# Kernel optimization log

Measured on AMD Instinct MI355X. Metric: run time of the kernel, lower is better.

## Reference

```python
import jax, jax.numpy as jnp
import numpy as np

N_NODES = 2048
D = 1024
B = 16384
E = 65536

def setup_inputs() -> dict:
    key = jax.random.key(0)
    ks = jax.random.split(key, 8)
    feat = jax.random.normal(ks[0], (B, 7, D), dtype=jnp.float32)
    data_x = jax.random.randint(ks[1], (7 * B,), 0, N_NODES, dtype=jnp.int64)
    adj_rows = jnp.sort(jax.random.randint(ks[2], (E,), 0, N_NODES, dtype=jnp.int32))
    adj_cols = jax.random.randint(ks[3], (E,), 0, N_NODES, dtype=jnp.int32)
    adj_vals = jax.random.uniform(ks[4], (E,), dtype=jnp.float32)
    # kaiming-uniform-like init for GCN weights, zero bias (as in reset_parameters)
    def kaiming(k, fan_in, fan_out):
        bound = jnp.sqrt(6.0 / fan_in)
        return jax.random.uniform(k, (fan_in, fan_out), minval=-bound, maxval=bound, dtype=jnp.float32)
    W1 = kaiming(ks[5], D, N_NODES)
    W2 = kaiming(ks[6], N_NODES, N_NODES)
    W3 = kaiming(ks[7], N_NODES, D)
    return {"feat": feat, "data_x": data_x, "adj_rows": adj_rows, "adj_cols": adj_cols,
            "adj_vals": adj_vals, "W1": W1, "b1": jnp.zeros((N_NODES,), jnp.float32),
            "W2": W2, "b2": jnp.zeros((N_NODES,), jnp.float32),
            "W3": W3, "b3": jnp.zeros((D,), jnp.float32)}

def reference(feat, data_x, adj_rows, adj_cols, adj_vals, W1, b1, W2, b2, W3, b3):
    n = b1.shape[0]  # number of nodes N
    e1 = data_x[0::7]  # [B]
    e2 = data_x[1::7]  # [B]
    # scatter-add: adjacency_matrix[e1] += feat[i,0]; adjacency_matrix[e2] += feat[i,1]
    idx = jnp.concatenate([e1, e2])                       # [2B]
    vals = jnp.concatenate([feat[:, 0, :], feat[:, 1, :]])  # [2B, D]
    node_feat = jax.ops.segment_sum(vals, idx, num_segments=n)  # [N, D]

    def spmm(x):  # sparse [N,N] @ dense [N,F]
        return jax.ops.segment_sum(adj_vals[:, None] * x[adj_cols], adj_rows, num_segments=n)

    h = jax.nn.relu(spmm(node_feat @ W1) + b1)  # [N, N]
    h = spmm(h @ W2) + b2                        # [N, N]
    logits = spmm(h @ W3) + b3                   # [N, D]

    # gather then swap: feat[:,0]=logits[e2], feat[:,1]=logits[e1]
    out = jnp.concatenate([logits[e2][:, None, :], logits[e1][:, None, :], feat[:, 2:, :]], axis=1)
    return out
```

## Files before the change

kernel.cpp:

```cpp
#include <hip/hip_runtime.h>
#include <stdint.h>

#define N_NODES 2048
#define DIM 1024
#define BATCH 16384
#define NEDGE 65536
#define CAP 96

typedef __bf16 bf16x8 __attribute__((ext_vector_type(8)));
typedef float f32x4 __attribute__((ext_vector_type(4)));
typedef unsigned short u16;
typedef unsigned int u32;

__device__ __forceinline__ float bf2f(u16 u) {
  union { u32 i; float f; } v; v.i = ((u32)u) << 16; return v.f;
}
__device__ __forceinline__ u16 f2bf(float f) {
  union { float f; u32 i; } v; v.f = f;
  u32 r = v.i + 0x7fffu + ((v.i >> 16) & 1u);
  return (u16)(r >> 16);
}

__global__ void k_detect(const int* __restrict__ dx, int* __restrict__ flag,
                         int* __restrict__ counts) {
  int t = threadIdx.x;
  for (int j = t; j < N_NODES; j += 64) counts[j] = 0;
  if (t == 0) {
    int is64 = 1;
    for (int j = 0; j < 32; ++j)
      if (dx[2 * j + 1] != 0) { is64 = 0; break; }
    *flag = is64;
  }
}

__global__ __launch_bounds__(256) void k_bucket(const int* __restrict__ dx,
                                                const int* __restrict__ flag,
                                                int* __restrict__ counts,
                                                int* __restrict__ bucket) {
  int i = blockIdx.x * 256 + threadIdx.x;
  if (i >= 2 * BATCH) return;
  int f = *flag;
  long p = (i < BATCH) ? 7L * i : 7L * (i - BATCH) + 1;
  int n = dx[f ? 2 * p : p] & (N_NODES - 1);
  int slot = atomicAdd(&counts[n], 1);
  if (slot < CAP) bucket[n * CAP + slot] = i;
}

__global__ __launch_bounds__(256) void k_nodesum(const float* __restrict__ feat,
                                                 const int* __restrict__ counts,
                                                 const int* __restrict__ bucket,
                                                 u16* __restrict__ A1) {
  int n = blockIdx.x;
  int tid = threadIdx.x;
  int cnt = counts[n]; if (cnt > CAP) cnt = CAP;
  float a0 = 0.f, a1 = 0.f, a2 = 0.f, a3 = 0.f;
  for (int j = 0; j < cnt; ++j) {
    int i = bucket[n * CAP + j];
    size_t rowoff = (i < BATCH) ? ((size_t)i * 7) * DIM
                                : ((size_t)(i - BATCH) * 7 + 1) * DIM;
    f32x4 v = *(const f32x4*)(feat + rowoff + tid * 4);
    a0 += v[0]; a1 += v[1]; a2 += v[2]; a3 += v[3];
  }
  ushort4 o; o.x = f2bf(a0); o.y = f2bf(a1); o.z = f2bf(a2); o.w = f2bf(a3);
  *(ushort4*)(A1 + (size_t)n * DIM + tid * 4) = o;
}

__global__ __launch_bounds__(256) void k_transpose(const float* __restrict__ W,
                                                   u16* __restrict__ Wt,
                                                   int K, int N) {
  __shared__ __align__(16) u16 t[32][33];
  int ntx = N >> 5;
  int bx = blockIdx.x % ntx;
  int by = blockIdx.x / ntx;
  int tx = threadIdx.x & 31, ty = threadIdx.x >> 5;
  #pragma unroll
  for (int r = 0; r < 32; r += 8)
    t[r + ty][tx] = f2bf(W[(size_t)(by * 32 + r + ty) * N + bx * 32 + tx]);
  __syncthreads();
  #pragma unroll
  for (int r = 0; r < 32; r += 8)
    Wt[(size_t)(bx * 32 + r + ty) * K + by * 32 + tx] = t[tx][r + ty];
}

__global__ __launch_bounds__(256) void k_rowptr(const int* __restrict__ adj_rows,
                                                int* __restrict__ row_ptr) {
  int r = blockIdx.x * 256 + threadIdx.x;
  if (r > N_NODES) return;
  int lo = 0, hi = NEDGE;
  while (lo < hi) { int mid = (lo + hi) >> 1; if (adj_rows[mid] < r) lo = mid + 1; else hi = mid; }
  row_ptr[r] = lo;
}

__global__ __launch_bounds__(256) void k_spmm(const u16* __restrict__ X16,
                                              const int* __restrict__ row_ptr,
                                              const int* __restrict__ adj_cols,
                                              const float* __restrict__ adj_vals,
                                              const float* __restrict__ bias,
                                              u16* __restrict__ Y16,
                                              float* __restrict__ Y32,
                                              int width) {
  int chunks = width >> 10;
  int ch = blockIdx.x % chunks;
  int r = blockIdx.x / chunks;
  int col = ch * 1024 + threadIdx.x * 4;
  int e0 = row_ptr[r], e1 = row_ptr[r + 1];
  float a0 = 0.f, a1 = 0.f, a2 = 0.f, a3 = 0.f;
  int e = e0;
  for (; e + 2 <= e1; e += 2) {
    int c0 = adj_cols[e] & (N_NODES - 1);
    int c1 = adj_cols[e + 1] & (N_NODES - 1);
    float v0 = adj_vals[e], v1 = adj_vals[e + 1];
    ushort4 x0 = *(const ushort4*)(X16 + (size_t)c0 * width + col);
    ushort4 x1 = *(const ushort4*)(X16 + (size_t)c1 * width + col);
    a0 += v0 * bf2f(x0.x) + v1 * bf2f(x1.x);
    a1 += v0 * bf2f(x0.y) + v1 * bf2f(x1.y);
    a2 += v0 * bf2f(x0.z) + v1 * bf2f(x1.z);
    a3 += v0 * bf2f(x0.w) + v1 * bf2f(x1.w);
  }
  if (e < e1) {
    int c = adj_cols[e] & (N_NODES - 1);
    float v = adj_vals[e];
    ushort4 x = *(const ushort4*)(X16 + (size_t)c * width + col);
    a0 += v * bf2f(x.x); a1 += v * bf2f(x.y);
    a2 += v * bf2f(x.z); a3 += v * bf2f(x.w);
  }
  if (Y16) {
    ushort4 o; o.x = f2bf(a0); o.y = f2bf(a1); o.z = f2bf(a2); o.w = f2bf(a3);
    *(ushort4*)(Y16 + (size_t)r * width + col) = o;
  } else {
    f32x4 bb = *(const f32x4*)(bias + col);
    f32x4 o; o[0] = a0 + bb[0]; o[1] = a1 + bb[1]; o[2] = a2 + bb[2]; o[3] = a3 + bb[3];
    *(f32x4*)(Y32 + (size_t)r * width + col) = o;
  }
}

template <int BM, int BN, bool BIAS, bool RELU>
__global__ __launch_bounds__(256) void k_gemm(const u16* __restrict__ A,
                                              const u16* __restrict__ Bt,
                                              const float* __restrict__ bias,
                                              u16* __restrict__ C16,
                                              int M, int N, int K) {
  constexpr int BK = 64;
  constexpr int WM = BM / 2, WN = BN / 2;
  constexpr int MI = WM / 16, NI = WN / 16;
  constexpr int IA = BM / 32, IB = BN / 32;
  __shared__ __align__(16) u16 As[2][BM * BK];
  __shared__ __align__(16) u16 Bs[2][BN * BK];
  const int ntx = N / BN;
  const int bx = blockIdx.x % ntx;
  const int by = blockIdx.x / ntx;
  const int tid = threadIdx.x;
  const int wid = tid >> 6;
  const int lane = tid & 63;
  const int wr = wid >> 1, wc = wid & 1;
  const int rowbase = by * BM, colbase = bx * BN;

  f32x4 acc[MI][NI];
  #pragma unroll
  for (int i = 0; i < MI; ++i)
    #pragma unroll
    for (int j = 0; j < NI; ++j) acc[i][j] = (f32x4){0.f, 0.f, 0.f, 0.f};

  const int srow = tid >> 3;
  const int skk = (((tid & 7) ^ (srow & 7)) << 3);

  #define STAGE(buf, kt)                                                        \
    do {                                                                        \
      _Pragma("unroll")                                                         \
      for (int i = 0; i < IA; ++i) {                                            \
        const u16* g = A + (size_t)(rowbase + i * 32 + srow) * K + (kt) + skk;  \
        __builtin_amdgcn_global_load_lds(                                       \
            (const __attribute__((address_space(1))) u32*)g,                    \
            (__attribute__((address_space(3))) u32*)(&As[buf][i * 2048 + tid * 8]), \
            16, 0, 0);                                                          \
      }                                                                         \
      _Pragma("unroll")                                                         \
      for (int i = 0; i < IB; ++i) {                                            \
        const u16* g = Bt + (size_t)(colbase + i * 32 + srow) * K + (kt) + skk; \
        __builtin_amdgcn_global_load_lds(                                       \
            (const __attribute__((address_space(1))) u32*)g,                    \
            (__attribute__((address_space(3))) u32*)(&Bs[buf][i * 2048 + tid * 8]), \
            16, 0, 0);                                                          \
      }                                                                         \
    } while (0)

  const int rrow = lane & 15;
  const int kq = (lane >> 4) * 8;
  const int rswz = (lane & 7) << 3;

  const int nk = K >> 6;
  STAGE(0, 0);
  __syncthreads();

  for (int t = 0; t < nk; ++t) {
    const u16* as = As[t & 1];
    const u16* bs = Bs[t & 1];
    if (t + 1 < nk) STAGE((t + 1) & 1, (t + 1) << 6);
    bf16x8 af[MI][2], bfr[NI][2];
    #pragma unroll
    for (int mi = 0; mi < MI; ++mi) {
      int r = wr * WM + mi * 16 + rrow;
      #pragma unroll
      for (int h = 0; h < 2; ++h)
        af[mi][h] = *(const bf16x8*)(as + r * 64 + ((h * 32 + kq) ^ rswz));
    }
    #pragma unroll
    for (int ni = 0; ni < NI; ++ni) {
      int c = wc * WN + ni * 16 + rrow;
      #pragma unroll
      for (int h = 0; h < 2; ++h)
        bfr[ni][h] = *(const bf16x8*)(bs + c * 64 + ((h * 32 + kq) ^ rswz));
    }
    #pragma unroll
    for (int h = 0; h < 2; ++h)
      #pragma unroll
      for (int mi = 0; mi < MI; ++mi)
        #pragma unroll
        for (int ni = 0; ni < NI; ++ni)
          acc[mi][ni] = __builtin_amdgcn_mfma_f32_16x16x32_bf16(af[mi][h], bfr[ni][h], acc[mi][ni], 0, 0, 0);
    __syncthreads();
  }
  #undef STAGE

  #pragma unroll
  for (int mi = 0; mi < MI; ++mi) {
    #pragma unroll
    for (int ni = 0; ni < NI; ++ni) {
      int col = colbase + wc * WN + ni * 16 + rrow;
      float bv = BIAS ? bias[col] : 0.f;
      #pragma unroll
      for (int j = 0; j < 4; ++j) {
        int row = rowbase + wr * WM + mi * 16 + (lane >> 4) * 4 + j;
        float v = acc[mi][ni][j] + bv;
        if (RELU) v = fmaxf(v, 0.f);
        C16[(size_t)row * N + col] = f2bf(v);
      }
    }
  }
}

__global__ __launch_bounds__(256) void k_assemble(const float* __restrict__ feat,
                                                  const float* __restrict__ logits,
                                                  const int* __restrict__ dx,
                                                  const int* __restrict__ flag,
                                                  float* __restrict__ out) {
  int i = blockIdx.x;
  int b = i / 7, slot = i - b * 7;
  const float* src;
  if (slot <= 1) {
    int f = *flag;
    long p = 7L * b + (slot == 0 ? 1 : 0);
    int node = dx[f ? 2 * p : p] & (N_NODES - 1);
    src = logits + (size_t)node * DIM;
  } else {
    src = feat + ((size_t)b * 7 + slot) * DIM;
  }
  f32x4 v = *(const f32x4*)(src + threadIdx.x * 4);
  __builtin_nontemporal_store(v, (f32x4*)(out + ((size_t)b * 7 + slot) * DIM + threadIdx.x * 4));
}

extern "C" void kernel_launch(void* const* d_in, const int* in_sizes, int n_in,
                              void* d_out, int out_size, void* d_ws, size_t ws_size,
                              hipStream_t stream) {
  const float* feat   = (const float*)d_in[0];
  const int* data_x   = (const int*)d_in[1];
  const int* adj_rows = (const int*)d_in[2];
  const int* adj_cols = (const int*)d_in[3];
  const float* adj_vals = (const float*)d_in[4];
  const float* W1 = (const float*)d_in[5];
  const float* b1 = (const float*)d_in[6];
  const float* W2 = (const float*)d_in[7];
  const float* b2 = (const float*)d_in[8];
  const float* W3 = (const float*)d_in[9];
  const float* b3 = (const float*)d_in[10];
  float* out = (float*)d_out;

  char* ws = (char*)d_ws;
  size_t off = 0;
  auto alloc = [&](size_t bytes) {
    char* p = ws + off; off += (bytes + 511) & ~(size_t)511; return p;
  };
  int*  flag    = (int*)alloc(4);
  int*  counts  = (int*)alloc(N_NODES * 4);
  int*  bucket  = (int*)alloc((size_t)N_NODES * CAP * 4);
  int*  row_ptr = (int*)alloc((N_NODES + 1) * 4);
  u16*  A1      = (u16*)alloc((size_t)N_NODES * DIM * 2);
  u16*  S       = (u16*)alloc((size_t)N_NODES * N_NODES * 2);
  u16*  H       = (u16*)alloc((size_t)N_NODES * N_NODES * 2);
  u16*  X3      = (u16*)alloc((size_t)N_NODES * DIM * 2);
  u16*  Wt      = (u16*)alloc((size_t)N_NODES * N_NODES * 2);
  float* logits = (float*)alloc((size_t)N_NODES * DIM * 4);

  k_detect<<<1, 64, 0, stream>>>(data_x, flag, counts);
  k_bucket<<<(2 * BATCH + 255) / 256, 256, 0, stream>>>(data_x, flag, counts, bucket);
  k_nodesum<<<N_NODES, 256, 0, stream>>>(feat, counts, bucket, A1);
  k_rowptr<<<N_NODES / 256 + 1, 256, 0, stream>>>(adj_rows, row_ptr);

  k_transpose<<<(N_NODES / 32) * (DIM / 32), 256, 0, stream>>>(W1, Wt, DIM, N_NODES);
  k_spmm<<<N_NODES * (DIM / 1024), 256, 0, stream>>>(A1, row_ptr, adj_cols, adj_vals, nullptr, S, nullptr, DIM);
  k_gemm<128, 64, true, true><<<(N_NODES / 128) * (N_NODES / 64), 256, 0, stream>>>(S, Wt, b1, H, N_NODES, N_NODES, DIM);
  k_transpose<<<(N_NODES / 32) * (N_NODES / 32), 256, 0, stream>>>(W2, Wt, N_NODES, N_NODES);
  k_spmm<<<N_NODES * (N_NODES / 1024), 256, 0, stream>>>(H, row_ptr, adj_cols, adj_vals, nullptr, S, nullptr, N_NODES);
  k_gemm<128, 64, true, false><<<(N_NODES / 128) * (N_NODES / 64), 256, 0, stream>>>(S, Wt, b2, H, N_NODES, N_NODES, N_NODES);
  k_transpose<<<(DIM / 32) * (N_NODES / 32), 256, 0, stream>>>(W3, Wt, N_NODES, DIM);
  k_gemm<64, 64, false, false><<<(N_NODES / 64) * (DIM / 64), 256, 0, stream>>>(H, Wt, nullptr, X3, N_NODES, DIM, N_NODES);
  k_spmm<<<N_NODES * (DIM / 1024), 256, 0, stream>>>(X3, row_ptr, adj_cols, adj_vals, b3, nullptr, logits, DIM);

  k_assemble<<<BATCH * 7, 256, 0, stream>>>(feat, logits, data_x, flag, out);
}
```

Before: 322.9 us.

## Overlap feat passthrough copy with GEMM/SpMM kernels and scatter logits directly

Splits the passthrough copy of feat slots 2..6 into chunks that extra blocks appended to each GEMM and SpMM launch perform. This overlaps that memory-bound work with the compute-bound kernels. The final SpMM writes logits straight into the output rows through the node buckets, which removes the logits buffer and the gather pass. Row_ptr is folded into k_detect, and the three weight transposes are merged into one launch with separate buffers. The risk is that copy blocks compete for bandwidth and CU slots with the main kernels, and the bucket CAP cap could drop rows if any node has more than 96 hits.

```diff
diff --git a/kernel.cpp b/kernel.cpp
--- a/kernel.cpp
+++ b/kernel.cpp
@@ -21,15 +21,35 @@
   return (u16)(r >> 16);
 }
 
-__global__ void k_detect(const int* __restrict__ dx, int* __restrict__ flag,
-                         int* __restrict__ counts) {
+__device__ __forceinline__ void copy_feat_rows(const float* __restrict__ feat,
+                                               float* __restrict__ out,
+                                               int row0, int tid) {
+  #pragma unroll 4
+  for (int t = row0; t < row0 + 32; ++t) {
+    int b = t / 5, s = t - b * 5 + 2;
+    size_t o = ((size_t)b * 7 + s) * DIM + tid * 4;
+    f32x4 v = __builtin_nontemporal_load((const f32x4*)(feat + o));
+    __builtin_nontemporal_store(v, (f32x4*)(out + o));
+  }
+}
+
+__global__ __launch_bounds__(256) void k_detect(const int* __restrict__ dx,
+                                                const int* __restrict__ adj_rows,
+                                                int* __restrict__ flag,
+                                                int* __restrict__ counts,
+                                                int* __restrict__ row_ptr) {
   int t = threadIdx.x;
-  for (int j = t; j < N_NODES; j += 64) counts[j] = 0;
+  for (int j = t; j < N_NODES; j += 256) counts[j] = 0;
   if (t == 0) {
     int is64 = 1;
     for (int j = 0; j < 32; ++j)
       if (dx[2 * j + 1] != 0) { is64 = 0; break; }
     *flag = is64;
+  }
+  for (int r = t; r <= N_NODES; r += 256) {
+    int lo = 0, hi = NEDGE;
+    while (lo < hi) { int mid = (lo + hi) >> 1; if (adj_rows[mid] < r) lo = mid + 1; else hi = mid; }
+    row_ptr[r] = lo;
   }
 }
 
@@ -65,13 +85,21 @@
   *(ushort4*)(A1 + (size_t)n * DIM + tid * 4) = o;
 }
 
-__global__ __launch_bounds__(256) void k_transpose(const float* __restrict__ W,
-                                                   u16* __restrict__ Wt,
-                                                   int K, int N) {
+__global__ __launch_bounds__(256) void k_transpose3(const float* __restrict__ W1,
+                                                    const float* __restrict__ W2,
+                                                    const float* __restrict__ W3,
+                                                    u16* __restrict__ Wt1,
+                                                    u16* __restrict__ Wt2,
+                                                    u16* __restrict__ Wt3) {
   __shared__ __align__(16) u16 t[32][33];
+  int bid = blockIdx.x;
+  const float* W; u16* Wt; int K, N, tb;
+  if (bid < 2048)      { W = W1; Wt = Wt1; K = DIM;     N = N_NODES; tb = bid; }
+  else if (bid < 6144) { W = W2; Wt = Wt2; K = N_NODES; N = N_NODES; tb = bid - 2048; }
+  else                 { W = W3; Wt = Wt3; K = N_NODES; N = DIM;     tb = bid - 6144; }
   int ntx = N >> 5;
-  int bx = blockIdx.x % ntx;
-  int by = blockIdx.x / ntx;
+  int bx = tb % ntx;
+  int by = tb / ntx;
   int tx = threadIdx.x & 31, ty = threadIdx.x >> 5;
   #pragma unroll
   for (int r = 0; r < 32; r += 8)
@@ -82,23 +110,22 @@
     Wt[(size_t)(bx * 32 + r + ty) * K + by * 32 + tx] = t[tx][r + ty];
 }
 
-__global__ __launch_bounds__(256) void k_rowptr(const int* __restrict__ adj_rows,
-                                                int* __restrict__ row_ptr) {
-  int r = blockIdx.x * 256 + threadIdx.x;
-  if (r > N_NODES) return;
-  int lo = 0, hi = NEDGE;
-  while (lo < hi) { int mid = (lo + hi) >> 1; if (adj_rows[mid] < r) lo = mid + 1; else hi = mid; }
-  row_ptr[r] = lo;
-}
-
+template <bool SCATTER>
 __global__ __launch_bounds__(256) void k_spmm(const u16* __restrict__ X16,
                                               const int* __restrict__ row_ptr,
                                               const int* __restrict__ adj_cols,
                                               const float* __restrict__ adj_vals,
                                               const float* __restrict__ bias,
                                               u16* __restrict__ Y16,
-                                              float* __restrict__ Y32,
-                                              int width) {
+                                              const int* __restrict__ counts,
+                                              const int* __restrict__ bucket,
+                                              const float* __restrict__ feat,
+                                              float* __restrict__ out,
+                                              int width, int ns, int crow0) {
+  if ((int)blockIdx.x >= ns) {
+    copy_feat_rows(feat, out, crow0 + ((int)blockIdx.x - ns) * 32, threadIdx.x);
+    return;
+  }
   int chunks = width >> 10;
   int ch = blockIdx.x % chunks;
   int r = blockIdx.x / chunks;
@@ -124,13 +151,18 @@
     a0 += v * bf2f(x.x); a1 += v * bf2f(x.y);
     a2 += v * bf2f(x.z); a3 += v * bf2f(x.w);
   }
-  if (Y16) {
+  if (SCATTER) {
+    f32x4 bb = *(const f32x4*)(bias + col);
+    f32x4 o; o[0] = a0 + bb[0]; o[1] = a1 + bb[1]; o[2] = a2 + bb[2]; o[3] = a3 + bb[3];
+    int cnt = counts[r]; if (cnt > CAP) cnt = CAP;
+    for (int j = 0; j < cnt; ++j) {
+      int i = bucket[r * CAP + j];
+      size_t p = (i < BATCH) ? ((size_t)i * 7 + 1) : ((size_t)(i - BATCH) * 7);
+      __builtin_nontemporal_store(o, (f32x4*)(out + p * DIM + col));
+    }
+  } else {
     ushort4 o; o.x = f2bf(a0); o.y = f2bf(a1); o.z = f2bf(a2); o.w = f2bf(a3);
     *(ushort4*)(Y16 + (size_t)r * width + col) = o;
-  } else {
-    f32x4 bb = *(const f32x4*)(bias + col);
-    f32x4 o; o[0] = a0 + bb[0]; o[1] = a1 + bb[1]; o[2] = a2 + bb[2]; o[3] = a3 + bb[3];
-    *(f32x4*)(Y32 + (size_t)r * width + col) = o;
   }
 }
 
@@ -139,13 +171,20 @@
                                               const u16* __restrict__ Bt,
                                               const float* __restrict__ bias,
                                               u16* __restrict__ C16,
-                                              int M, int N, int K) {
+                                              const float* __restrict__ feat,
+                                              float* __restrict__ out,
+                                              int M, int N, int K,
+                                              int ng, int crow0) {
   constexpr int BK = 64;
   constexpr int WM = BM / 2, WN = BN / 2;
   constexpr int MI = WM / 16, NI = WN / 16;
   constexpr int IA = BM / 32, IB = BN / 32;
   __shared__ __align__(16) u16 As[2][BM * BK];
   __shared__ __align__(16) u16 Bs[2][BN * BK];
+  if ((int)blockIdx.x >= ng) {
+    copy_feat_rows(feat, out, crow0 + ((int)blockIdx.x - ng) * 32, threadIdx.x);
+    return;
+  }
   const int ntx = N / BN;
   const int bx = blockIdx.x % ntx;
   const int by = blockIdx.x / ntx;
@@ -239,24 +278,9 @@
   }
 }
 
-__global__ __launch_bounds__(256) void k_assemble(const float* __restrict__ feat,
-                                                  const float* __restrict__ logits,
-                                                  const int* __restrict__ dx,
-                                                  const int* __restrict__ flag,
-                                                  float* __restrict__ out) {
-  int i = blockIdx.x;
-  int b = i / 7, slot = i - b * 7;
-  const float* src;
-  if (slot <= 1) {
-    int f = *flag;
-    long p = 7L * b + (slot == 0 ? 1 : 0);
-    int node = dx[f ? 2 * p : p] & (N_NODES - 1);
-    src = logits + (size_t)node * DIM;
-  } else {
-    src = feat + ((size_t)b * 7 + slot) * DIM;
-  }
-  f32x4 v = *(const f32x4*)(src + threadIdx.x * 4);
-  __builtin_nontemporal_store(v, (f32x4*)(out + ((size_t)b * 7 + slot) * DIM + threadIdx.x * 4));
+__global__ __launch_bounds__(256) void k_copy(const float* __restrict__ feat,
+                                              float* __restrict__ out, int crow0) {
+  copy_feat_rows(feat, out, crow0 + blockIdx.x * 32, threadIdx.x);
 }
 
 extern "C" void kernel_launch(void* const* d_in, const int* in_sizes, int n_in,
@@ -288,23 +312,27 @@
   u16*  S       = (u16*)alloc((size_t)N_NODES * N_NODES * 2);
   u16*  H       = (u16*)alloc((size_t)N_NODES * N_NODES * 2);
   u16*  X3      = (u16*)alloc((size_t)N_NODES * DIM * 2);
-  u16*  Wt      = (u16*)alloc((size_t)N_NODES * N_NODES * 2);
-  float* logits = (float*)alloc((size_t)N_NODES * DIM * 4);
-
-  k_detect<<<1, 64, 0, stream>>>(data_x, flag, counts);
+  u16*  Wt1     = (u16*)alloc((size_t)DIM * N_NODES * 2);
+  u16*  Wt2     = (u16*)alloc((size_t)N_NODES * N_NODES * 2);
+  u16*  Wt3     = (u16*)alloc((size_t)N_NODES * DIM * 2);
+
+  k_detect<<<1, 256, 0, stream>>>(data_x, adj_rows, flag, counts, row_ptr);
   k_bucket<<<(2 * BATCH + 255) / 256, 256, 0, stream>>>(data_x, flag, counts, bucket);
   k_nodesum<<<N_NODES, 256, 0, stream>>>(feat, counts, bucket, A1);
-  k_rowptr<<<N_NODES / 256 + 1, 256, 0, stream>>>(adj_rows, row_ptr);
-
-  k_transpose<<<(N_NODES / 32) * (DIM / 32), 256, 0, stream>>>(W1, Wt, DIM, N_NODES);
-  k_spmm<<<N_NODES * (DIM / 1024), 256, 0, stream>>>(A1, row_ptr, adj_cols, adj_vals, nullptr, S, nullptr, DIM);
-  k_gemm<128, 64, true, true><<<(N_NODES / 128) * (N_NODES / 64), 256, 0, stream>>>(S, Wt, b1, H, N_NODES, N_NODES, DIM);
-  k_transpose<<<(N_NODES / 32) * (N_NODES / 32), 256, 0, stream>>>(W2, Wt, N_NODES, N_NODES);
-  k_spmm<<<N_NODES * (N_NODES / 1024), 256, 0, stream>>>(H, row_ptr, adj_cols, adj_vals, nullptr, S, nullptr, N_NODES);
-  k_gemm<128, 64, true, false><<<(N_NODES / 128) * (N_NODES / 64), 256, 0, stream>>>(S, Wt, b2, H, N_NODES, N_NODES, N_NODES);
-  k_transpose<<<(DIM / 32) * (N_NODES / 32), 256, 0, stream>>>(W3, Wt, N_NODES, DIM);
-  k_gemm<64, 64, false, false><<<(N_NODES / 64) * (DIM / 64), 256, 0, stream>>>(H, Wt, nullptr, X3, N_NODES, DIM, N_NODES);
-  k_spmm<<<N_NODES * (DIM / 1024), 256, 0, stream>>>(X3, row_ptr, adj_cols, adj_vals, b3, nullptr, logits, DIM);
-
-  k_assemble<<<BATCH * 7, 256, 0, stream>>>(feat, logits, data_x, flag, out);
-}
+  k_transpose3<<<8192, 256, 0, stream>>>(W1, W2, W3, Wt1, Wt2, Wt3);
+
+  k_spmm<false><<<2048 + 256, 256, 0, stream>>>(A1, row_ptr, adj_cols, adj_vals, nullptr, S,
+                                                nullptr, nullptr, feat, out, DIM, 2048, 49152);
+  k_gemm<128, 64, true, true><<<512 + 512, 256, 0, stream>>>(S, Wt1, b1, H, feat, out,
+                                                             N_NODES, N_NODES, DIM, 512, 0);
+  k_spmm<false><<<4096 + 256, 256, 0, stream>>>(H, row_ptr, adj_cols, adj_vals, nullptr, S,
+                                                nullptr, nullptr, feat, out, N_NODES, 4096, 57344);
+  k_gemm<128, 64, true, false><<<512 + 512, 256, 0, stream>>>(S, Wt2, b2, H, feat, out,
+                                                              N_NODES, N_NODES, N_NODES, 512, 16384);
+  k_gemm<64, 64, false, false><<<512 + 512, 256, 0, stream>>>(H, Wt3, nullptr, X3, feat, out,
+                                                              N_NODES, DIM, N_NODES, 512, 32768);
+  k_spmm<true><<<2048 + 256, 256, 0, stream>>>(X3, row_ptr, adj_cols, adj_vals, b3, nullptr,
+                                               counts, bucket, feat, out, DIM, 2048, 65536);
+
+  k_copy<<<256, 256, 0, stream>>>(feat, out, 73728);
+}
```

New measurement: 341.7 us. 5.8% more time.

## Merge preprocessing kernels into one launch and enlarge GEMM tiles

Applied to the files above, without the earlier changes.

Folds the int64-format detection into the bucketing kernel and replaces the counts-zeroing with a memset. The node sum, row-pointer search and all three weight transposes now run in one combined kernel, writing to three separate transposed-weight buffers. The first two GEMMs move to 128x128 tiles with 512 threads, and the third to 128x64 tiles. This removes several launches and serialisation points and should improve GEMM data reuse, at the cost of extra workspace and fewer, larger GEMM blocks.

```diff
diff --git a/kernel.cpp b/kernel.cpp
--- a/kernel.cpp
+++ b/kernel.cpp
@@ -21,58 +21,69 @@
   return (u16)(r >> 16);
 }
 
-__global__ void k_detect(const int* __restrict__ dx, int* __restrict__ flag,
-                         int* __restrict__ counts) {
-  int t = threadIdx.x;
-  for (int j = t; j < N_NODES; j += 64) counts[j] = 0;
-  if (t == 0) {
-    int is64 = 1;
-    for (int j = 0; j < 32; ++j)
-      if (dx[2 * j + 1] != 0) { is64 = 0; break; }
-    *flag = is64;
-  }
-}
-
 __global__ __launch_bounds__(256) void k_bucket(const int* __restrict__ dx,
-                                                const int* __restrict__ flag,
+                                                int* __restrict__ flag,
                                                 int* __restrict__ counts,
                                                 int* __restrict__ bucket) {
+  int is64 = 1;
+  for (int j = 0; j < 32; ++j)
+    if (dx[2 * j + 1] != 0) { is64 = 0; break; }
+  if (blockIdx.x == 0 && threadIdx.x == 0) *flag = is64;
   int i = blockIdx.x * 256 + threadIdx.x;
   if (i >= 2 * BATCH) return;
-  int f = *flag;
   long p = (i < BATCH) ? 7L * i : 7L * (i - BATCH) + 1;
-  int n = dx[f ? 2 * p : p] & (N_NODES - 1);
+  int n = dx[is64 ? 2 * p : p] & (N_NODES - 1);
   int slot = atomicAdd(&counts[n], 1);
   if (slot < CAP) bucket[n * CAP + slot] = i;
 }
 
-__global__ __launch_bounds__(256) void k_nodesum(const float* __restrict__ feat,
-                                                 const int* __restrict__ counts,
-                                                 const int* __restrict__ bucket,
-                                                 u16* __restrict__ A1) {
-  int n = blockIdx.x;
+__global__ __launch_bounds__(256) void k_prep2(const float* __restrict__ feat,
+                                               const int* __restrict__ counts,
+                                               const int* __restrict__ bucket,
+                                               u16* __restrict__ A1,
+                                               const int* __restrict__ adj_rows,
+                                               int* __restrict__ row_ptr,
+                                               const float* __restrict__ W1,
+                                               const float* __restrict__ W2,
+                                               const float* __restrict__ W3,
+                                               u16* __restrict__ Wt1,
+                                               u16* __restrict__ Wt2,
+                                               u16* __restrict__ Wt3) {
+  __shared__ __align__(16) u16 t[32][33];
+  int bid = blockIdx.x;
   int tid = threadIdx.x;
-  int cnt = counts[n]; if (cnt > CAP) cnt = CAP;
-  float a0 = 0.f, a1 = 0.f, a2 = 0.f, a3 = 0.f;
-  for (int j = 0; j < cnt; ++j) {
-    int i = bucket[n * CAP + j];
-    size_t rowoff = (i < BATCH) ? ((size_t)i * 7) * DIM
-                                : ((size_t)(i - BATCH) * 7 + 1) * DIM;
-    f32x4 v = *(const f32x4*)(feat + rowoff + tid * 4);
-    a0 += v[0]; a1 += v[1]; a2 += v[2]; a3 += v[3];
-  }
-  ushort4 o; o.x = f2bf(a0); o.y = f2bf(a1); o.z = f2bf(a2); o.w = f2bf(a3);
-  *(ushort4*)(A1 + (size_t)n * DIM + tid * 4) = o;
-}
-
-__global__ __launch_bounds__(256) void k_transpose(const float* __restrict__ W,
-                                                   u16* __restrict__ Wt,
-                                                   int K, int N) {
-  __shared__ __align__(16) u16 t[32][33];
+  if (bid < 2048) {
+    int n = bid;
+    int cnt = counts[n]; if (cnt > CAP) cnt = CAP;
+    float a0 = 0.f, a1 = 0.f, a2 = 0.f, a3 = 0.f;
+    for (int j = 0; j < cnt; ++j) {
+      int i = bucket[n * CAP + j];
+      size_t rowoff = (i < BATCH) ? ((size_t)i * 7) * DIM
+                                  : ((size_t)(i - BATCH) * 7 + 1) * DIM;
+      f32x4 v = *(const f32x4*)(feat + rowoff + tid * 4);
+      a0 += v[0]; a1 += v[1]; a2 += v[2]; a3 += v[3];
+    }
+    ushort4 o; o.x = f2bf(a0); o.y = f2bf(a1); o.z = f2bf(a2); o.w = f2bf(a3);
+    *(ushort4*)(A1 + (size_t)n * DIM + tid * 4) = o;
+    return;
+  }
+  if (bid < 2057) {
+    int r = (bid - 2048) * 256 + tid;
+    if (r > N_NODES) return;
+    int lo = 0, hi = NEDGE;
+    while (lo < hi) { int mid = (lo + hi) >> 1; if (adj_rows[mid] < r) lo = mid + 1; else hi = mid; }
+    row_ptr[r] = lo;
+    return;
+  }
+  int tb = bid - 2057;
+  const float* W; u16* Wt; int K, N;
+  if (tb < 2048)      { W = W1; Wt = Wt1; K = DIM;     N = N_NODES; }
+  else if (tb < 6144) { W = W2; Wt = Wt2; K = N_NODES; N = N_NODES; tb -= 2048; }
+  else                { W = W3; Wt = Wt3; K = N_NODES; N = DIM;     tb -= 6144; }
   int ntx = N >> 5;
-  int bx = blockIdx.x % ntx;
-  int by = blockIdx.x / ntx;
-  int tx = threadIdx.x & 31, ty = threadIdx.x >> 5;
+  int bx = tb % ntx;
+  int by = tb / ntx;
+  int tx = tid & 31, ty = tid >> 5;
   #pragma unroll
   for (int r = 0; r < 32; r += 8)
     t[r + ty][tx] = f2bf(W[(size_t)(by * 32 + r + ty) * N + bx * 32 + tx]);
@@ -82,15 +93,7 @@
     Wt[(size_t)(bx * 32 + r + ty) * K + by * 32 + tx] = t[tx][r + ty];
 }
 
-__global__ __launch_bounds__(256) void k_rowptr(const int* __restrict__ adj_rows,
-                                                int* __restrict__ row_ptr) {
-  int r = blockIdx.x * 256 + threadIdx.x;
-  if (r > N_NODES) return;
-  int lo = 0, hi = NEDGE;
-  while (lo < hi) { int mid = (lo + hi) >> 1; if (adj_rows[mid] < r) lo = mid + 1; else hi = mid; }
-  row_ptr[r] = lo;
-}
-
+template <bool F32OUT>
 __global__ __launch_bounds__(256) void k_spmm(const u16* __restrict__ X16,
                                               const int* __restrict__ row_ptr,
                                               const int* __restrict__ adj_cols,
@@ -124,26 +127,28 @@
     a0 += v * bf2f(x.x); a1 += v * bf2f(x.y);
     a2 += v * bf2f(x.z); a3 += v * bf2f(x.w);
   }
-  if (Y16) {
-    ushort4 o; o.x = f2bf(a0); o.y = f2bf(a1); o.z = f2bf(a2); o.w = f2bf(a3);
-    *(ushort4*)(Y16 + (size_t)r * width + col) = o;
-  } else {
+  if (F32OUT) {
     f32x4 bb = *(const f32x4*)(bias + col);
     f32x4 o; o[0] = a0 + bb[0]; o[1] = a1 + bb[1]; o[2] = a2 + bb[2]; o[3] = a3 + bb[3];
     *(f32x4*)(Y32 + (size_t)r * width + col) = o;
-  }
-}
-
-template <int BM, int BN, bool BIAS, bool RELU>
-__global__ __launch_bounds__(256) void k_gemm(const u16* __restrict__ A,
-                                              const u16* __restrict__ Bt,
-                                              const float* __restrict__ bias,
-                                              u16* __restrict__ C16,
-                                              int M, int N, int K) {
+  } else {
+    ushort4 o; o.x = f2bf(a0); o.y = f2bf(a1); o.z = f2bf(a2); o.w = f2bf(a3);
+    *(ushort4*)(Y16 + (size_t)r * width + col) = o;
+  }
+}
+
+template <int BM, int BN, int THREADS, bool BIAS, bool RELU>
+__global__ __launch_bounds__(THREADS) void k_gemm(const u16* __restrict__ A,
+                                                  const u16* __restrict__ Bt,
+                                                  const float* __restrict__ bias,
+                                                  u16* __restrict__ C16,
+                                                  int M, int N, int K) {
   constexpr int BK = 64;
-  constexpr int WM = BM / 2, WN = BN / 2;
+  constexpr int WAVES_N = THREADS / 128;
+  constexpr int WM = BM / 2, WN = BN / WAVES_N;
   constexpr int MI = WM / 16, NI = WN / 16;
-  constexpr int IA = BM / 32, IB = BN / 32;
+  constexpr int RPI = THREADS / 8;
+  constexpr int IA = BM / RPI, IB = BN / RPI;
   __shared__ __align__(16) u16 As[2][BM * BK];
   __shared__ __align__(16) u16 Bs[2][BN * BK];
   const int ntx = N / BN;
@@ -152,7 +157,7 @@
   const int tid = threadIdx.x;
   const int wid = tid >> 6;
   const int lane = tid & 63;
-  const int wr = wid >> 1, wc = wid & 1;
+  const int wr = wid / WAVES_N, wc = wid % WAVES_N;
   const int rowbase = by * BM, colbase = bx * BN;
 
   f32x4 acc[MI][NI];
@@ -168,18 +173,18 @@
     do {                                                                        \
       _Pragma("unroll")                                                         \
       for (int i = 0; i < IA; ++i) {                                            \
-        const u16* g = A + (size_t)(rowbase + i * 32 + srow) * K + (kt) + skk;  \
+        const u16* g = A + (size_t)(rowbase + i * RPI + srow) * K + (kt) + skk; \
         __builtin_amdgcn_global_load_lds(                                       \
             (const __attribute__((address_space(1))) u32*)g,                    \
-            (__attribute__((address_space(3))) u32*)(&As[buf][i * 2048 + tid * 8]), \
+            (__attribute__((address_space(3))) u32*)(&As[buf][i * (RPI * 64) + tid * 8]), \
             16, 0, 0);                                                          \
       }                                                                         \
       _Pragma("unroll")                                                         \
       for (int i = 0; i < IB; ++i) {                                            \
-        const u16* g = Bt + (size_t)(colbase + i * 32 + srow) * K + (kt) + skk; \
+        const u16* g = Bt + (size_t)(colbase + i * RPI + srow) * K + (kt) + skk;\
         __builtin_amdgcn_global_load_lds(                                       \
             (const __attribute__((address_space(1))) u32*)g,                    \
-            (__attribute__((address_space(3))) u32*)(&Bs[buf][i * 2048 + tid * 8]), \
+            (__attribute__((address_space(3))) u32*)(&Bs[buf][i * (RPI * 64) + tid * 8]), \
             16, 0, 0);                                                          \
       }                                                                         \
     } while (0)
@@ -288,23 +293,25 @@
   u16*  S       = (u16*)alloc((size_t)N_NODES * N_NODES * 2);
   u16*  H       = (u16*)alloc((size_t)N_NODES * N_NODES * 2);
   u16*  X3      = (u16*)alloc((size_t)N_NODES * DIM * 2);
-  u16*  Wt      = (u16*)alloc((size_t)N_NODES * N_NODES * 2);
+  u16*  Wt1     = (u16*)alloc((size_t)DIM * N_NODES * 2);
+  u16*  Wt2     = (u16*)alloc((size_t)N_NODES * N_NODES * 2);
+  u16*  Wt3     = (u16*)alloc((size_t)N_NODES * DIM * 2);
   float* logits = (float*)alloc((size_t)N_NODES * DIM * 4);
 
-  k_detect<<<1, 64, 0, stream>>>(data_x, flag, counts);
+  hipMemsetAsync(counts, 0, N_NODES * 4, stream);
   k_bucket<<<(2 * BATCH + 255) / 256, 256, 0, stream>>>(data_x, flag, counts, bucket);
-  k_nodesum<<<N_NODES, 256, 0, stream>>>(feat, counts, bucket, A1);
-  k_rowptr<<<N_NODES / 256 + 1, 256, 0, stream>>>(adj_rows, row_ptr);
-
-  k_transpose<<<(N_NODES / 32) * (DIM / 32), 256, 0, stream>>>(W1, Wt, DIM, N_NODES);
-  k_spmm<<<N_NODES * (DIM / 1024), 256, 0, stream>>>(A1, row_ptr, adj_cols, adj_vals, nullptr, S, nullptr, DIM);
-  k_gemm<128, 64, true, true><<<(N_NODES / 128) * (N_NODES / 64), 256, 0, stream>>>(S, Wt, b1, H, N_NODES, N_NODES, DIM);
-  k_transpose<<<(N_NODES / 32) * (N_NODES / 32), 256, 0, stream>>>(W2, Wt, N_NODES, N_NODES);
-  k_spmm<<<N_NODES * (N_NODES / 1024), 256, 0, stream>>>(H, row_ptr, adj_cols, adj_vals, nullptr, S, nullptr, N_NODES);
-  k_gemm<128, 64, true, false><<<(N_NODES / 128) * (N_NODES / 64), 256, 0, stream>>>(S, Wt, b2, H, N_NODES, N_NODES, N_NODES);
-  k_transpose<<<(DIM / 32) * (N_NODES / 32), 256, 0, stream>>>(W3, Wt, N_NODES, DIM);
-  k_gemm<64, 64, false, false><<<(N_NODES / 64) * (DIM / 64), 256, 0, stream>>>(H, Wt, nullptr, X3, N_NODES, DIM, N_NODES);
-  k_spmm<<<N_NODES * (DIM / 1024), 256, 0, stream>>>(X3, row_ptr, adj_cols, adj_vals, b3, nullptr, logits, DIM);
+  k_prep2<<<2057 + 8192, 256, 0, stream>>>(feat, counts, bucket, A1, adj_rows, row_ptr,
+                                           W1, W2, W3, Wt1, Wt2, Wt3);
+
+  k_spmm<false><<<2048, 256, 0, stream>>>(A1, row_ptr, adj_cols, adj_vals, nullptr, S,
+                                          nullptr, DIM);
+  k_gemm<128, 128, 512, true, true><<<256, 512, 0, stream>>>(S, Wt1, b1, H, N_NODES, N_NODES, DIM);
+  k_spmm<false><<<4096, 256, 0, stream>>>(H, row_ptr, adj_cols, adj_vals, nullptr, S,
+                                          nullptr, N_NODES);
+  k_gemm<128, 128, 512, true, false><<<256, 512, 0, stream>>>(S, Wt2, b2, H, N_NODES, N_NODES, N_NODES);
+  k_gemm<128, 64, 256, false, false><<<256, 256, 0, stream>>>(H, Wt3, nullptr, X3, N_NODES, DIM, N_NODES);
+  k_spmm<true><<<2048, 256, 0, stream>>>(X3, row_ptr, adj_cols, adj_vals, b3, nullptr,
+                                         logits, DIM);
 
   k_assemble<<<BATCH * 7, 256, 0, stream>>>(feat, logits, data_x, flag, out);
 }
```

Result: no change. 317.6 us, median of 2 (-1.6%).
